# Performance work log

Hardware: AMD Instinct MI355X
Metric: run time of the kernel (lower is better)

Reference implementation:

```python
import jax, jax.numpy as jnp
import numpy as np

TIMELEN = 2016   # 288*7
T1 = 288         # steps per day
T3 = 864         # 288*3 time-graph nodes
LBAND = 3        # band width of time adjacency
N = 325          # input_dim = number of sensors
H = 325          # hidden_dim = num_nodes (conv channels)
B = 32
KSIZE = 577


def _norm_adj():
    # geneTimeAdj(864, L): banded time adjacency, symmetric, incl. self-loop
    i = np.arange(T3)
    A = (np.abs(i[:, None] - i[None, :]) <= LBAND).astype(np.float32)
    d = A.sum(1) ** -0.5
    return jnp.asarray(d[:, None] * A * d[None, :])  # D^-1/2 A D^-1/2


def setup_inputs() -> dict:
    key = jax.random.key(0)
    ks = jax.random.split(key, 12)

    def kaiming(k, fan_in, shape):
        bound = float(np.sqrt(6.0 / fan_in))
        return jax.random.uniform(k, shape, jnp.float32, -bound, bound)

    inp = {
        'input_feature': jax.random.normal(ks[0], (B, N, T1), jnp.float32),
        'x': jax.random.normal(ks[1], (TIMELEN, N), jnp.float32),  # standardized KB
        'w1': kaiming(ks[2], N, (N, H)), 'b1': jnp.zeros((H,), jnp.float32),
        'w11': kaiming(ks[3], H, (H, H)), 'b11': jnp.zeros((H,), jnp.float32),
        'w2': kaiming(ks[4], H, (H, H)), 'b2': jnp.zeros((H,), jnp.float32),
        'w22': kaiming(ks[5], H, (H, H)), 'b22': jnp.zeros((H,), jnp.float32),
        'w3': kaiming(ks[6], H, (H, H)), 'b3': jnp.zeros((H,), jnp.float32),
        'w33': kaiming(ks[7], H, (H, H)), 'b33': jnp.zeros((H,), jnp.float32),
        'conv_w': kaiming(ks[8], H * KSIZE, (H, H, KSIZE)),  # Conv1d(H->H, k=577)
        'conv_b': jnp.zeros((H,), jnp.float32),
        'week': jax.random.randint(ks[9], (B,), 0, 7, jnp.int32),
        'hour': jax.random.randint(ks[10], (B,), 0, T1, jnp.int32),
    }
    return inp


def reference(input_feature, x, w1, b1, w11, b11, w2, b2, w22, b22,
              w3, b3, w33, b33, conv_w, conv_b, week, hour):
    A = _norm_adj()
    c0 = jnp.concatenate([jnp.eye(T1, dtype=jnp.float32),
                          jnp.zeros((TIMELEN - T1, T1), jnp.float32)], 0)
    c10 = jnp.concatenate([jnp.eye(T3, dtype=jnp.float32),
                           jnp.zeros((TIMELEN - T3, T3), jnp.float32)], 0)
    shift = week * T1 + hour                      # per-sample circshift
    c = jax.vmap(lambda s: jnp.roll(c0, s, axis=0))(shift)        # [B,TL,288]
    c1 = jax.vmap(lambda s: jnp.roll(c10, s - T1, axis=0))(shift)  # [B,TL,864]

    cTx = jnp.einsum('btk,td->bkd', c, x)                          # [B,288,N]
    cin = jnp.einsum('btk,bkd->btd', c,
                     jnp.transpose(input_feature, (0, 2, 1)) - cTx)  # [B,TL,N]
    temp = jnp.einsum('btm,btd->bmd', c1, x + cin)                  # [B,864,N]

    def gcn(feat, w, b):
        support = jnp.einsum('bnd,do->bno', feat, w)
        return jnp.einsum('mn,bno->bmo', A, support) + b

    out = jnp.tanh(gcn(temp, w1, b1)) * jax.nn.sigmoid(gcn(temp, w11, b11))
    out = jnp.tanh(gcn(out, w2, b2)) * jax.nn.sigmoid(gcn(out, w22, b22))
    out = jnp.tanh(gcn(out, w3, b3)) * jax.nn.sigmoid(gcn(out, w33, b33))

    out = jnp.transpose(out, (0, 2, 1))  # [B,H,864]
    out = jax.lax.conv_general_dilated(
        out, conv_w, window_strides=(1,), padding='VALID',
        dimension_numbers=('NCH', 'OIH', 'NCH'))
    return out + conv_b[None, :, None]   # [B,H,288]
```

## Files before the change

kernel.cpp:

```cpp
#include <hip/hip_runtime.h>


typedef _Float16 half8 __attribute__((ext_vector_type(8)));
typedef float floatx4 __attribute__((ext_vector_type(4)));

#define DEV __device__ __forceinline__
#define AS1 __attribute__((address_space(1)))
#define AS3 __attribute__((address_space(3)))

constexpr int IPAD = 352;
constexpr int NPAD = 384;
constexpr int MGCN = 32 * 864;
constexpr int MCONV = 32 * 288;
constexpr int KCONV_PAD = 203136;
constexpr int CONV_SPLITS = 6;
constexpr int CH32_TOTAL = KCONV_PAD / 32;
constexpr int CH32_SPLIT = CH32_TOTAL / CONV_SPLITS;

constexpr size_t OFF_XG = 0;
constexpr size_t SZ_XG_AL = 19465216;
constexpr size_t SZ_S = (size_t)MGCN * NPAD * 4;
constexpr size_t OFF_S1 = OFF_XG + SZ_XG_AL;
constexpr size_t OFF_S2 = OFF_S1 + SZ_S;
constexpr size_t OFF_WG = OFF_S2 + SZ_S;
constexpr size_t SZ_WG = 6ull * NPAD * NPAD * 2;
constexpr size_t OFF_WCONV = OFF_WG + SZ_WG;
constexpr size_t OFF_CPART = OFF_S1;

DEV void gload16(const void* g, void* l) {
    __builtin_amdgcn_global_load_lds((const AS1 void*)g, (AS3 void*)l, 16, 0, 0);
}

#define MEMFENCE() asm volatile("" ::: "memory")
#define BARRIER() do { MEMFENCE(); __builtin_amdgcn_s_barrier(); MEMFENCE(); } while (0)

__global__ void k_temp(const float* __restrict__ IF, const float* __restrict__ x,
                       const int* __restrict__ week, const int* __restrict__ hour,
                       _Float16* __restrict__ Xg) {
    int idx = blockIdx.x * 256 + threadIdx.x;
    if (idx >= MGCN * IPAD) return;
    int i  = idx % IPAD;
    int mm = idx / IPAD;
    int m  = mm % 864, b = mm / 864;
    float v = 0.f;
    if (i < 325) {
        if (m >= 288 && m < 576) {
            v = IF[((size_t)b * 325 + i) * 288 + (m - 288)];
        } else {
            int s  = week[b] * 288 + hour[b];
            int tm = (m + s + 1728) % 2016;
            v = x[(size_t)tm * 325 + i];
        }
    }
    Xg[(size_t)mm * IPAD + i] = (_Float16)v;
}

__global__ void k_pack_gcn(const float* w0, const float* w1, const float* w2,
                           const float* w3, const float* w4, const float* w5,
                           _Float16* __restrict__ Wg) {
    int idx = blockIdx.x * 256 + threadIdx.x;
    int d = idx % NPAD;
    int o = (idx / NPAD) % NPAD;
    int l = idx / (NPAD * NPAD);
    const float* w = l == 0 ? w0 : l == 1 ? w1 : l == 2 ? w2 : l == 3 ? w3 : l == 4 ? w4 : w5;
    float v = (o < 325 && d < 325) ? w[d * 325 + o] : 0.f;
    Wg[(size_t)idx] = (_Float16)v;
}

__global__ void k_pack_conv(const float* __restrict__ cw, _Float16* __restrict__ Wc) {
    __shared__ float tile[32][33];
    int o = blockIdx.x, i0 = blockIdx.y * 32, k0 = blockIdx.z * 32;
    int t = threadIdx.x;
    int c = t & 31, r4 = t >> 5;
#pragma unroll
    for (int p = 0; p < 4; ++p) {
        int ii = r4 * 4 + p;
        int i = i0 + ii, k = k0 + c;
        float v = 0.f;
        if (o < 325 && i < 325 && k < 577) v = cw[((size_t)o * 325 + i) * 577 + k];
        tile[ii][c] = v;
    }
    __syncthreads();
#pragma unroll
    for (int p = 0; p < 4; ++p) {
        int kk = r4 * 4 + p;
        int k = k0 + kk, i = i0 + c;
        int kidx = k * IPAD + i;
        if (kidx < KCONV_PAD) Wc[(size_t)o * KCONV_PAD + kidx] = (_Float16)tile[c][kk];
    }
}

template <bool CONV>
__global__ __launch_bounds__(256) void k_gemm(const _Float16* __restrict__ Xg,
                                              const _Float16* __restrict__ Bw,
                                              float* __restrict__ C,
                                              int bStride, int chunksPerSplit,
                                              int chunksTotal, long long sliceStride) {
    __shared__ _Float16 sA[128 * 64];
    __shared__ _Float16 sB[128 * 64];
    const int t = threadIdx.x;
    const int m0 = blockIdx.x * 128, n0 = blockIdx.y * 128;
    const int bz = blockIdx.z;
    int chunk0 = bz * chunksPerSplit;
    int nch = chunksTotal - chunk0;
    if (nch > chunksPerSplit) nch = chunksPerSplit;
    C += (size_t)bz * (size_t)sliceStride;

    const int rj = t >> 3;
    const int cg = (t & 7) ^ (rj & 7);
    const _Float16* pa[4];
    const _Float16* pb[4];
#pragma unroll
    for (int j = 0; j < 4; ++j) {
        int m = m0 + j * 32 + rj;
        int mrow = CONV ? (m + (m / 288) * 576) : m;
        pa[j] = Xg + (size_t)mrow * IPAD + (size_t)chunk0 * 64 + cg * 8;
        int n = n0 + j * 32 + rj;
        pb[j] = Bw + (size_t)n * bStride + (size_t)chunk0 * 64 + cg * 8;
    }

    const int lane = t & 63, wv = t >> 6;
    const int wm = wv >> 1, wn = wv & 1;
    const int r = lane & 15, q = lane >> 4, s8 = r & 7;
    int aRow[4], bRow[4];
#pragma unroll
    for (int i = 0; i < 4; ++i) {
        aRow[i] = (wm * 64 + i * 16 + r) * 64;
        bRow[i] = (wn * 64 + i * 16 + r) * 64;
    }
    const int xk0 = (q ^ s8) * 8;
    const int xk1 = ((q + 4) ^ s8) * 8;

    floatx4 acc[4][4] = {};

    for (int ch = 0; ch < nch; ++ch) {
        __syncthreads();
#pragma unroll
        for (int j = 0; j < 4; ++j) { gload16(pa[j], &sA[(j * 256 + t) * 8]); pa[j] += 64; }
#pragma unroll
        for (int j = 0; j < 4; ++j) { gload16(pb[j], &sB[(j * 256 + t) * 8]); pb[j] += 64; }
        __syncthreads();
#pragma unroll
        for (int kk = 0; kk < 2; ++kk) {
            const int xk = kk ? xk1 : xk0;
            half8 av[4], bv[4];
#pragma unroll
            for (int mi = 0; mi < 4; ++mi) av[mi] = *(const half8*)(sA + aRow[mi] + xk);
#pragma unroll
            for (int ni = 0; ni < 4; ++ni) bv[ni] = *(const half8*)(sB + bRow[ni] + xk);
#pragma unroll
            for (int mi = 0; mi < 4; ++mi)
#pragma unroll
                for (int ni = 0; ni < 4; ++ni)
                    acc[mi][ni] = __builtin_amdgcn_mfma_f32_16x16x32_f16(av[mi], bv[ni],
                                                                         acc[mi][ni], 0, 0, 0);
        }
    }

#pragma unroll
    for (int mi = 0; mi < 4; ++mi)
#pragma unroll
        for (int ni = 0; ni < 4; ++ni) {
            int row = m0 + wm * 64 + mi * 16 + q * 4;
            int col = n0 + wn * 64 + ni * 16 + r;
#pragma unroll
            for (int e = 0; e < 4; ++e)
                C[(size_t)(row + e) * NPAD + col] = acc[mi][ni][e];
        }
}

__global__ __launch_bounds__(512, 2) void k_conv(const _Float16* __restrict__ Xg,
                                                 const _Float16* __restrict__ Wc,
                                                 float* __restrict__ C) {
    __shared__ _Float16 lds[3 * 20480];
    const int t = threadIdx.x;
    const int m0 = blockIdx.x * 256;
    const int z  = blockIdx.y;
    const int chunk0 = z * CH32_SPLIT;
    const int nch = CH32_SPLIT;
    C += (size_t)z * MCONV * NPAD;

    const _Float16* src[5];
    int ldsoff[5];
#pragma unroll
    for (int p = 0; p < 2; ++p) {
        int s = t + p * 512;
        int j = s >> 3, cc = s & 7;
        int g = cc ^ (j & 7);
        int m = m0 + 2 * j + (g >> 2);
        int mrow = m + (m / 288) * 576;
        src[p] = Xg + (size_t)mrow * IPAD + (size_t)chunk0 * 32 + (g & 3) * 8;
        ldsoff[p] = s * 16;
    }
#pragma unroll
    for (int p = 0; p < 3; ++p) {
        int s = t + p * 512;
        int j = s >> 3, cc = s & 7;
        int g = cc ^ (j & 7);
        int n = 2 * j + (g >> 2);
        src[2 + p] = Wc + (size_t)n * KCONV_PAD + (size_t)chunk0 * 32 + (g & 3) * 8;
        ldsoff[2 + p] = 16384 + s * 16;
    }

    const int lane = t & 63, wv = t >> 6;
    const int wm = wv >> 1, wn = wv & 1;
    const int r = lane & 15, q = lane >> 4;
    int row_a = wm * 64 + r;
    int aoff0 = (row_a >> 1) * 128 + ((((row_a & 1) << 2) | q) ^ ((row_a >> 1) & 7)) * 16;
    int row_b = wn * 192 + r;
    int boff0 = 16384 + (row_b >> 1) * 128 +
                ((((row_b & 1) << 2) | q) ^ ((row_b >> 1) & 7)) * 16;

    floatx4 acc[4][12] = {};

    auto stage = [&](int lc, int buf) {
        char* dst = (char*)lds + buf * 40960;
        size_t adv = (size_t)lc * 32;
#pragma unroll
        for (int p = 0; p < 5; ++p)
            gload16(src[p] + adv, dst + ldsoff[p]);
    };

    stage(0, 0);
    stage(1, 1);

    int buf = 0;
    for (int lc = 0; lc < nch; ++lc) {
        int pre = lc + 2;  if (pre > nch - 1) pre = nch - 1;
        int pbuf = buf + 2; if (pbuf >= 3) pbuf -= 3;
        stage(pre, pbuf);
        asm volatile("s_waitcnt vmcnt(10)" ::: "memory");
        BARRIER();
        const char* cb = (const char*)lds + buf * 40960;
        half8 av[4];
#pragma unroll
        for (int mi = 0; mi < 4; ++mi)
            av[mi] = *(const half8*)(cb + aoff0 + mi * 1024);
#pragma unroll
        for (int ni = 0; ni < 12; ++ni) {
            half8 bv = *(const half8*)(cb + boff0 + ni * 1024);
#pragma unroll
            for (int mi = 0; mi < 4; ++mi)
                acc[mi][ni] = __builtin_amdgcn_mfma_f32_16x16x32_f16(av[mi], bv,
                                                                     acc[mi][ni], 0, 0, 0);
        }
        BARRIER();
        buf = (buf + 1 == 3) ? 0 : buf + 1;
    }
    asm volatile("s_waitcnt vmcnt(0)" ::: "memory");

#pragma unroll
    for (int mi = 0; mi < 4; ++mi)
#pragma unroll
        for (int ni = 0; ni < 12; ++ni) {
            int row = m0 + wm * 64 + mi * 16 + q * 4;
            int col = wn * 192 + ni * 16 + r;
#pragma unroll
            for (int e = 0; e < 4; ++e)
                C[(size_t)(row + e) * NPAD + col] = acc[mi][ni][e];
        }
}

__global__ void k_bandact(const float* __restrict__ S1, const float* __restrict__ S2,
                          const float* __restrict__ b1, const float* __restrict__ b2,
                          _Float16* __restrict__ Xg) {
    int bm = blockIdx.x;
    int m = bm % 864;
    int dm = (m < 3 ? m : 3) + ((863 - m) < 3 ? (863 - m) : 3) + 1;
    for (int o = threadIdx.x; o < 325; o += 256) {
        float g1 = b1[o], g2 = b2[o];
#pragma unroll
        for (int dn = -3; dn <= 3; ++dn) {
            int n = m + dn;
            if (n < 0 || n > 863) continue;
            int dnd = (n < 3 ? n : 3) + ((863 - n) < 3 ? (863 - n) : 3) + 1;
            float a = rsqrtf((float)(dm * dnd));
            size_t off = (size_t)(bm + dn) * NPAD + o;
            g1 += a * S1[off];
            g2 += a * S2[off];
        }
        float vt = tanhf(g1);
        float vs = 1.f / (1.f + expf(-g2));
        Xg[(size_t)bm * IPAD + o] = (_Float16)(vt * vs);
    }
}

__global__ void k_reduce(const float* __restrict__ Cp, const float* __restrict__ cb,
                         float* __restrict__ out) {
    __shared__ float tile[32][33];
    int b = blockIdx.x, t0 = blockIdx.y * 32, o0 = blockIdx.z * 32;
    int t = threadIdx.x;
    int c = t & 31, r4 = t >> 5;
#pragma unroll
    for (int p = 0; p < 4; ++p) {
        int tt = r4 * 4 + p;
        size_t mrow = (size_t)(b * 288 + t0 + tt) * NPAD + (o0 + c);
        float acc = 0.f;
#pragma unroll
        for (int s = 0; s < CONV_SPLITS; ++s)
            acc += Cp[(size_t)s * MCONV * NPAD + mrow];
        tile[tt][c] = acc;
    }
    __syncthreads();
#pragma unroll
    for (int p = 0; p < 4; ++p) {
        int oo = r4 * 4 + p;
        int o = o0 + oo;
        if (o < 325)
            out[((size_t)b * 325 + o) * 288 + t0 + c] = tile[c][oo] + cb[o];
    }
}

extern "C" void kernel_launch(void* const* d_in, const int* in_sizes, int n_in,
                              void* d_out, int out_size, void* d_ws, size_t ws_size,
                              hipStream_t stream) {
    const float* IF = (const float*)d_in[0];
    const float* x  = (const float*)d_in[1];
    const float* wg[6] = {(const float*)d_in[2],  (const float*)d_in[4],
                          (const float*)d_in[6],  (const float*)d_in[8],
                          (const float*)d_in[10], (const float*)d_in[12]};
    const float* bg[6] = {(const float*)d_in[3],  (const float*)d_in[5],
                          (const float*)d_in[7],  (const float*)d_in[9],
                          (const float*)d_in[11], (const float*)d_in[13]};
    const float* cw  = (const float*)d_in[14];
    const float* cb  = (const float*)d_in[15];
    const int* week  = (const int*)d_in[16];
    const int* hour  = (const int*)d_in[17];
    float* out = (float*)d_out;

    char* ws = (char*)d_ws;
    _Float16* Xg = (_Float16*)(ws + OFF_XG);
    float* S1    = (float*)(ws + OFF_S1);
    float* S2    = (float*)(ws + OFF_S2);
    _Float16* Wg = (_Float16*)(ws + OFF_WG);
    _Float16* Wc = (_Float16*)(ws + OFF_WCONV);
    float* Cp    = (float*)(ws + OFF_CPART);

    k_pack_gcn<<<(6 * NPAD * NPAD) / 256, 256, 0, stream>>>(wg[0], wg[1], wg[2], wg[3],
                                                            wg[4], wg[5], Wg);
    k_pack_conv<<<dim3(NPAD, 11, 19), 256, 0, stream>>>(cw, Wc);
    k_temp<<<(MGCN * IPAD) / 256, 256, 0, stream>>>(IF, x, week, hour, Xg);

    for (int l = 0; l < 3; ++l) {
        k_gemm<false><<<dim3(MGCN / 128, NPAD / 128, 1), 256, 0, stream>>>(
            Xg, Wg + (size_t)(2 * l) * NPAD * NPAD, S1, NPAD, 6, 6, 0);
        k_gemm<false><<<dim3(MGCN / 128, NPAD / 128, 1), 256, 0, stream>>>(
            Xg, Wg + (size_t)(2 * l + 1) * NPAD * NPAD, S2, NPAD, 6, 6, 0);
        k_bandact<<<MGCN, 256, 0, stream>>>(S1, S2, bg[2 * l], bg[2 * l + 1], Xg);
    }

    k_conv<<<dim3(MCONV / 256, CONV_SPLITS), 512, 0, stream>>>(Xg, Wc, Cp);

    k_reduce<<<dim3(32, 9, 11), 256, 0, stream>>>(Cp, cb, out);
}
```

Baseline: 2.182 ms.

## Fuse paired GCN GEMMs into one launch and atomically reduce conv splits

```diff
diff --git a/kernel.cpp b/kernel.cpp
--- a/kernel.cpp
+++ b/kernel.cpp
@@ -10,22 +10,22 @@
 
 constexpr int IPAD = 352;
 constexpr int NPAD = 384;
+constexpr int NFUSE = 768;
 constexpr int MGCN = 32 * 864;
 constexpr int MCONV = 32 * 288;
 constexpr int KCONV_PAD = 203136;
-constexpr int CONV_SPLITS = 6;
+constexpr int CONV_SPLITS = 7;
 constexpr int CH32_TOTAL = KCONV_PAD / 32;
-constexpr int CH32_SPLIT = CH32_TOTAL / CONV_SPLITS;
+constexpr int CH32_PER = 907;
 
 constexpr size_t OFF_XG = 0;
 constexpr size_t SZ_XG_AL = 19465216;
-constexpr size_t SZ_S = (size_t)MGCN * NPAD * 4;
-constexpr size_t OFF_S1 = OFF_XG + SZ_XG_AL;
-constexpr size_t OFF_S2 = OFF_S1 + SZ_S;
-constexpr size_t OFF_WG = OFF_S2 + SZ_S;
+constexpr size_t OFF_S = OFF_XG + SZ_XG_AL;
+constexpr size_t SZ_S = (size_t)MGCN * NFUSE * 4;
+constexpr size_t OFF_WG = OFF_S + SZ_S;
 constexpr size_t SZ_WG = 6ull * NPAD * NPAD * 2;
 constexpr size_t OFF_WCONV = OFF_WG + SZ_WG;
-constexpr size_t OFF_CPART = OFF_S1;
+constexpr size_t OFF_CPART = OFF_S;
 
 DEV void gload16(const void* g, void* l) {
     __builtin_amdgcn_global_load_lds((const AS1 void*)g, (AS3 void*)l, 16, 0, 0);
@@ -90,21 +90,13 @@
     }
 }
 
-template <bool CONV>
 __global__ __launch_bounds__(256) void k_gemm(const _Float16* __restrict__ Xg,
                                               const _Float16* __restrict__ Bw,
-                                              float* __restrict__ C,
-                                              int bStride, int chunksPerSplit,
-                                              int chunksTotal, long long sliceStride) {
+                                              float* __restrict__ C) {
     __shared__ _Float16 sA[128 * 64];
     __shared__ _Float16 sB[128 * 64];
     const int t = threadIdx.x;
     const int m0 = blockIdx.x * 128, n0 = blockIdx.y * 128;
-    const int bz = blockIdx.z;
-    int chunk0 = bz * chunksPerSplit;
-    int nch = chunksTotal - chunk0;
-    if (nch > chunksPerSplit) nch = chunksPerSplit;
-    C += (size_t)bz * (size_t)sliceStride;
 
     const int rj = t >> 3;
     const int cg = (t & 7) ^ (rj & 7);
@@ -113,10 +105,9 @@
 #pragma unroll
     for (int j = 0; j < 4; ++j) {
         int m = m0 + j * 32 + rj;
-        int mrow = CONV ? (m + (m / 288) * 576) : m;
-        pa[j] = Xg + (size_t)mrow * IPAD + (size_t)chunk0 * 64 + cg * 8;
+        pa[j] = Xg + (size_t)m * IPAD + cg * 8;
         int n = n0 + j * 32 + rj;
-        pb[j] = Bw + (size_t)n * bStride + (size_t)chunk0 * 64 + cg * 8;
+        pb[j] = Bw + (size_t)n * NPAD + cg * 8;
     }
 
     const int lane = t & 63, wv = t >> 6;
@@ -133,7 +124,7 @@
 
     floatx4 acc[4][4] = {};
 
-    for (int ch = 0; ch < nch; ++ch) {
+    for (int ch = 0; ch < 6; ++ch) {
         __syncthreads();
 #pragma unroll
         for (int j = 0; j < 4; ++j) { gload16(pa[j], &sA[(j * 256 + t) * 8]); pa[j] += 64; }
@@ -165,7 +156,7 @@
             int col = n0 + wn * 64 + ni * 16 + r;
 #pragma unroll
             for (int e = 0; e < 4; ++e)
-                C[(size_t)(row + e) * NPAD + col] = acc[mi][ni][e];
+                C[(size_t)(row + e) * NFUSE + col] = acc[mi][ni][e];
         }
 }
 
@@ -175,10 +166,9 @@
     __shared__ _Float16 lds[3 * 20480];
     const int t = threadIdx.x;
     const int m0 = blockIdx.x * 256;
-    const int z  = blockIdx.y;
-    const int chunk0 = z * CH32_SPLIT;
-    const int nch = CH32_SPLIT;
-    C += (size_t)z * MCONV * NPAD;
+    const int chunk0 = blockIdx.y * CH32_PER;
+    int nch = CH32_TOTAL - chunk0;
+    if (nch > CH32_PER) nch = CH32_PER;
 
     const _Float16* src[5];
     int ldsoff[5];
@@ -257,11 +247,11 @@
             int col = wn * 192 + ni * 16 + r;
 #pragma unroll
             for (int e = 0; e < 4; ++e)
-                C[(size_t)(row + e) * NPAD + col] = acc[mi][ni][e];
-        }
-}
-
-__global__ void k_bandact(const float* __restrict__ S1, const float* __restrict__ S2,
+                unsafeAtomicAdd(&C[(size_t)(row + e) * NPAD + col], acc[mi][ni][e]);
+        }
+}
+
+__global__ void k_bandact(const float* __restrict__ S,
                           const float* __restrict__ b1, const float* __restrict__ b2,
                           _Float16* __restrict__ Xg) {
     int bm = blockIdx.x;
@@ -275,9 +265,9 @@
             if (n < 0 || n > 863) continue;
             int dnd = (n < 3 ? n : 3) + ((863 - n) < 3 ? (863 - n) : 3) + 1;
             float a = rsqrtf((float)(dm * dnd));
-            size_t off = (size_t)(bm + dn) * NPAD + o;
-            g1 += a * S1[off];
-            g2 += a * S2[off];
+            size_t off = (size_t)(bm + dn) * NFUSE + o;
+            g1 += a * S[off];
+            g2 += a * S[off + NPAD];
         }
         float vt = tanhf(g1);
         float vs = 1.f / (1.f + expf(-g2));
@@ -294,12 +284,7 @@
 #pragma unroll
     for (int p = 0; p < 4; ++p) {
         int tt = r4 * 4 + p;
-        size_t mrow = (size_t)(b * 288 + t0 + tt) * NPAD + (o0 + c);
-        float acc = 0.f;
-#pragma unroll
-        for (int s = 0; s < CONV_SPLITS; ++s)
-            acc += Cp[(size_t)s * MCONV * NPAD + mrow];
-        tile[tt][c] = acc;
+        tile[tt][c] = Cp[(size_t)(b * 288 + t0 + tt) * NPAD + (o0 + c)];
     }
     __syncthreads();
 #pragma unroll
@@ -330,8 +315,7 @@
 
     char* ws = (char*)d_ws;
     _Float16* Xg = (_Float16*)(ws + OFF_XG);
-    float* S1    = (float*)(ws + OFF_S1);
-    float* S2    = (float*)(ws + OFF_S2);
+    float* S     = (float*)(ws + OFF_S);
     _Float16* Wg = (_Float16*)(ws + OFF_WG);
     _Float16* Wc = (_Float16*)(ws + OFF_WCONV);
     float* Cp    = (float*)(ws + OFF_CPART);
@@ -342,13 +326,12 @@
     k_temp<<<(MGCN * IPAD) / 256, 256, 0, stream>>>(IF, x, week, hour, Xg);
 
     for (int l = 0; l < 3; ++l) {
-        k_gemm<false><<<dim3(MGCN / 128, NPAD / 128, 1), 256, 0, stream>>>(
-            Xg, Wg + (size_t)(2 * l) * NPAD * NPAD, S1, NPAD, 6, 6, 0);
-        k_gemm<false><<<dim3(MGCN / 128, NPAD / 128, 1), 256, 0, stream>>>(
-            Xg, Wg + (size_t)(2 * l + 1) * NPAD * NPAD, S2, NPAD, 6, 6, 0);
-        k_bandact<<<MGCN, 256, 0, stream>>>(S1, S2, bg[2 * l], bg[2 * l + 1], Xg);
-    }
-
+        k_gemm<<<dim3(MGCN / 128, NFUSE / 128), 256, 0, stream>>>(
+            Xg, Wg + (size_t)(2 * l) * NPAD * NPAD, S);
+        k_bandact<<<MGCN, 256, 0, stream>>>(S, bg[2 * l], bg[2 * l + 1], Xg);
+    }
+
+    hipMemsetAsync(Cp, 0, (size_t)MCONV * NPAD * 4, stream);
     k_conv<<<dim3(MCONV / 256, CONV_SPLITS), 512, 0, stream>>>(Xg, Wc, Cp);
 
     k_reduce<<<dim3(32, 9, 11), 256, 0, stream>>>(Cp, cb, out);
```

New measurement: 2.041 ms. 1.07x faster.
